# Optimization experiments

Measured on AMD Instinct MI355X. Metric: run time of the kernel, lower is better.

The kernel has to match this reference:

```python
import jax, jax.numpy as jnp
import numpy as np

N = 100000      # nodes
E = 1000000     # edges per relation
DIN = 64
DOUT = 64
NEG_SLOPE = 0.2  # DGL GATConv leaky_relu default


def setup_inputs() -> dict:
    key = jax.random.key(0)
    ks = jax.random.split(key, 16)
    inp = {"x": jax.random.normal(ks[0], (N, DIN), dtype=jnp.float32)}
    i = 1
    for rel in ("concur", "upd", "side"):
        inp[f"src_{rel}"] = jax.random.randint(ks[i], (E,), 0, N, dtype=jnp.int32); i += 1
        inp[f"dst_{rel}"] = jax.random.randint(ks[i], (E,), 0, N, dtype=jnp.int32); i += 1
        inp[f"W_{rel}"] = jax.random.normal(ks[i], (DIN, DOUT), dtype=jnp.float32) * 0.1; i += 1
        inp[f"al_{rel}"] = jax.random.normal(ks[i], (DOUT,), dtype=jnp.float32) * 0.1; i += 1
        inp[f"ar_{rel}"] = jax.random.normal(ks[i], (DOUT,), dtype=jnp.float32) * 0.1; i += 1
        inp[f"b_{rel}"] = jnp.zeros((DOUT,), dtype=jnp.float32)
    return inp


def _gat_rel(x, src, dst, W, al, ar, b, n):
    """Single-head DGL GATConv on one relation (homogeneous src/dst type)."""
    feat = x @ W                      # [N, DOUT] projected features
    el = feat @ al                    # [N] source attention logits
    er = feat @ ar                    # [N] destination attention logits
    e = el[src] + er[dst]             # [E]
    e = jnp.where(e > 0, e, NEG_SLOPE * e)  # leaky_relu
    # edge softmax normalized per destination node
    m = jax.ops.segment_max(e, dst, num_segments=n)
    a = jnp.exp(e - m[dst])
    s = jax.ops.segment_sum(a, dst, num_segments=n)
    a = a / s[dst]
    # scatter-weighted aggregation of source features onto destinations
    out = jax.ops.segment_sum(a[:, None] * feat[src], dst, num_segments=n)
    return out + b


def reference(x,
              src_concur, dst_concur, src_upd, dst_upd, src_side, dst_side,
              W_concur, al_concur, ar_concur, b_concur,
              W_upd, al_upd, ar_upd, b_upd,
              W_side, al_side, ar_side, b_side):
    n = x.shape[0]
    out = (_gat_rel(x, src_concur, dst_concur, W_concur, al_concur, ar_concur, b_concur, n)
           + _gat_rel(x, src_upd, dst_upd, W_upd, al_upd, ar_upd, b_upd, n)
           + _gat_rel(x, src_side, dst_side, W_side, al_side, ar_side, b_side, n))
    return out[:, None, :]  # [N, num_heads=1, DOUT] to match DGL GATConv output
```

## Files before the change

kernel.cpp:

```cpp
#include <hip/hip_runtime.h>

#define DIM 64
#define NEG 0.2f
#define SB 1024
#define RPW 8
#define BNODES 512
#define SHIFTB 9
#define NBMAX 1024
#define CHUNK 8192

__device__ __forceinline__ float rl(float v, int l) {
  return __int_as_float(__builtin_amdgcn_readlane(__float_as_int(v), l));
}

__device__ __forceinline__ unsigned short f2bf(float f) {
  unsigned u = __float_as_uint(f);
  u += 0x7FFFu + ((u >> 16) & 1u);
  return (unsigned short)(u >> 16);
}

__global__ __launch_bounds__(64) void prep_kernel(
    const float* __restrict__ W0, const float* __restrict__ W1, const float* __restrict__ W2,
    const float* __restrict__ al0, const float* __restrict__ ar0,
    const float* __restrict__ al1, const float* __restrict__ ar1,
    const float* __restrict__ al2, const float* __restrict__ ar2,
    const float* __restrict__ b0, const float* __restrict__ b1, const float* __restrict__ b2,
    float* __restrict__ q, float* __restrict__ bias) {
  int b = blockIdx.x, c = threadIdx.x;
  if (b < 6) {
    int rel = b >> 1;
    const float* W = rel == 0 ? W0 : (rel == 1 ? W1 : W2);
    const float* a;
    if (b & 1) a = rel == 0 ? ar0 : (rel == 1 ? ar1 : ar2);
    else       a = rel == 0 ? al0 : (rel == 1 ? al1 : al2);
    float s = 0.f;
#pragma unroll
    for (int j = 0; j < DIM; ++j) s = fmaf(W[c * DIM + j], a[j], s);
    q[b * DIM + c] = s;
  } else {
    bias[c] = b0[c] + b1[c] + b2[c];
  }
}

__global__ __launch_bounds__(256) void elr_kernel(
    const float* __restrict__ x, const float* __restrict__ q,
    float* __restrict__ el, float* __restrict__ er, int n) {
  __shared__ float Qs[6 * DIM];
  for (int i = threadIdx.x; i < 6 * DIM; i += 256) Qs[i] = q[i];
  __syncthreads();
  int i = blockIdx.x * blockDim.x + threadIdx.x;
  if (i >= n) return;
  const float4* x4 = (const float4*)x;
  const float4* Q4 = (const float4*)Qs;
  float a[6] = {0.f, 0.f, 0.f, 0.f, 0.f, 0.f};
#pragma unroll 4
  for (int t = 0; t < 16; ++t) {
    float4 xv = x4[(size_t)i * 16 + t];
#pragma unroll
    for (int j = 0; j < 6; ++j) {
      float4 qv = Q4[j * 16 + t];
      a[j] = fmaf(xv.x, qv.x, a[j]);
      a[j] = fmaf(xv.y, qv.y, a[j]);
      a[j] = fmaf(xv.z, qv.z, a[j]);
      a[j] = fmaf(xv.w, qv.w, a[j]);
    }
  }
#pragma unroll
  for (int r = 0; r < 3; ++r) {
    el[(size_t)r * n + i] = a[2 * r];
    er[(size_t)r * n + i] = a[2 * r + 1];
  }
}

__global__ __launch_bounds__(256) void proj3(
    const float* __restrict__ x,
    const float* __restrict__ W0, const float* __restrict__ W1, const float* __restrict__ W2,
    unsigned short* __restrict__ feat, int n) {
  __shared__ float WsP[3 * 4096];
  const int lane = threadIdx.x & 63;
  const int wv = threadIdx.x >> 6;
  for (int i = threadIdx.x; i < DIM * DIM; i += 256) {
    int k = i >> 6, c = i & 63;
    int d = (k >> 1) * 128 + c * 2 + (k & 1);
    WsP[d] = W0[i];
    WsP[4096 + d] = W1[i];
    WsP[8192 + d] = W2[i];
  }
  __syncthreads();

  const int rowbase = (blockIdx.x * 4 + wv) * RPW;
  float xr[RPW];
#pragma unroll
  for (int r = 0; r < RPW; ++r) {
    int row = rowbase + r;
    row = row < n ? row : n - 1;
    xr[r] = x[(size_t)row * DIM + lane];
  }
  float a0[RPW], a1[RPW], a2[RPW];
#pragma unroll
  for (int r = 0; r < RPW; ++r) { a0[r] = 0.f; a1[r] = 0.f; a2[r] = 0.f; }

  const float2* Wp0 = (const float2*)WsP;
  const float2* Wp1 = (const float2*)(WsP + 4096);
  const float2* Wp2 = (const float2*)(WsP + 8192);
#pragma unroll 8
  for (int k2 = 0; k2 < 32; ++k2) {
    float2 w0 = Wp0[k2 * 64 + lane];
    float2 w1 = Wp1[k2 * 64 + lane];
    float2 w2 = Wp2[k2 * 64 + lane];
#pragma unroll
    for (int r = 0; r < RPW; ++r) {
      float xv0 = rl(xr[r], 2 * k2);
      float xv1 = rl(xr[r], 2 * k2 + 1);
      a0[r] = fmaf(xv1, w0.y, fmaf(xv0, w0.x, a0[r]));
      a1[r] = fmaf(xv1, w1.y, fmaf(xv0, w1.x, a1[r]));
      a2[r] = fmaf(xv1, w2.y, fmaf(xv0, w2.x, a2[r]));
    }
  }
#pragma unroll
  for (int r = 0; r < RPW; ++r) {
    int row = rowbase + r;
    if (row < n) {
      feat[(size_t)row * DIM + lane] = f2bf(a0[r]);
      feat[((size_t)n + row) * DIM + lane] = f2bf(a1[r]);
      feat[((size_t)2 * n + row) * DIM + lane] = f2bf(a2[r]);
    }
  }
}

__global__ __launch_bounds__(256) void proj_kernel(
    const float* __restrict__ x, const float* __restrict__ W,
    const float* __restrict__ al, const float* __restrict__ ar,
    unsigned short* __restrict__ feat, float* __restrict__ el, float* __restrict__ er, int n) {
  __shared__ float Ws[DIM][DIM];
  int tid = threadIdx.y * 64 + threadIdx.x;
  for (int i = tid; i < DIM * DIM; i += 256) Ws[i >> 6][i & 63] = W[i];
  __syncthreads();
  int row = blockIdx.x * 4 + threadIdx.y;
  if (row >= n) return;
  int lane = threadIdx.x;
  const float* xr = x + (size_t)row * DIM;
  float acc = 0.f;
#pragma unroll
  for (int k = 0; k < DIM; ++k) acc = fmaf(xr[k], Ws[k][lane], acc);
  feat[(size_t)row * DIM + lane] = f2bf(acc);
  float pl = acc * al[lane], pr = acc * ar[lane];
#pragma unroll
  for (int o = 32; o > 0; o >>= 1) {
    pl += __shfl_xor(pl, o, 64);
    pr += __shfl_xor(pr, o, 64);
  }
  if (lane == 0) { el[row] = pl; er[row] = pr; }
}

__global__ void init_out(float* __restrict__ out,
                         const float* __restrict__ b0, const float* __restrict__ b1,
                         const float* __restrict__ b2, int n) {
  int i = blockIdx.x * blockDim.x + threadIdx.x;
  if (i < n * DIM) {
    int c = i & (DIM - 1);
    out[i] = b0[c] + b1[c] + b2[c];
  }
}

__global__ void count3(const int* __restrict__ d0, const int* __restrict__ d1,
                       const int* __restrict__ d2, int e0, int e1, int e2,
                       int* __restrict__ cnt, int n) {
  int i = blockIdx.x * blockDim.x + threadIdx.x;
  int r, li;
  const int* dp;
  if (i < e0)                { r = 0; li = i;           dp = d0; }
  else if (i < e0 + e1)      { r = 1; li = i - e0;      dp = d1; }
  else if (i < e0 + e1 + e2) { r = 2; li = i - e0 - e1; dp = d2; }
  else return;
  atomicAdd(&cnt[r * n + dp[li]], 1);
}

__global__ __launch_bounds__(SB) void scan1(const int* __restrict__ cnt, int* __restrict__ off,
                                            int* __restrict__ bsum, int n) {
  __shared__ int sm[SB];
  int i = blockIdx.x * SB + threadIdx.x;
  int v = (i < n) ? cnt[i] : 0;
  sm[threadIdx.x] = v;
  __syncthreads();
  for (int o = 1; o < SB; o <<= 1) {
    int t = ((int)threadIdx.x >= o) ? sm[threadIdx.x - o] : 0;
    __syncthreads();
    sm[threadIdx.x] += t;
    __syncthreads();
  }
  if (i < n) off[i + 1] = sm[threadIdx.x];
  if (threadIdx.x == SB - 1) bsum[blockIdx.x] = sm[SB - 1];
}

__global__ __launch_bounds__(SB) void scan2(int* __restrict__ bsum, int nb) {
  __shared__ int sm[SB];
  int v = ((int)threadIdx.x < nb) ? bsum[threadIdx.x] : 0;
  sm[threadIdx.x] = v;
  __syncthreads();
  for (int o = 1; o < SB; o <<= 1) {
    int t = ((int)threadIdx.x >= o) ? sm[threadIdx.x - o] : 0;
    __syncthreads();
    sm[threadIdx.x] += t;
    __syncthreads();
  }
  if ((int)threadIdx.x < nb) bsum[threadIdx.x] = sm[threadIdx.x] - v;
}

__global__ __launch_bounds__(SB) void scan3(int* __restrict__ off, const int* __restrict__ bsum,
                                            int n) {
  int i = blockIdx.x * SB + threadIdx.x;
  if (i < n) off[i + 1] += bsum[blockIdx.x];
  if (i == 0) off[0] = 0;
}

__global__ void init_bcur(const int* __restrict__ off, int* __restrict__ bcur, int nbuckets) {
  int b = blockIdx.x * blockDim.x + threadIdx.x;
  if (b < nbuckets) bcur[b] = off[b << SHIFTB];
}

__global__ __launch_bounds__(256) void bin3(
    const int* __restrict__ s0, const int* __restrict__ d0,
    const int* __restrict__ s1, const int* __restrict__ d1,
    const int* __restrict__ s2, const int* __restrict__ d2,
    int e0, int e1, int e2,
    const float* __restrict__ el, const float* __restrict__ er,
    int* __restrict__ bcur, int2* __restrict__ binPairs,
    unsigned short* __restrict__ binLoc, int n, int nbuckets) {
  __shared__ int hist[NBMAX];
  __shared__ int base[NBMAX];
  const int tot = e0 + e1 + e2;
  const int cbeg = blockIdx.x * CHUNK;
  const int cend = min(cbeg + CHUNK, tot);
  for (int b = threadIdx.x; b < nbuckets; b += 256) hist[b] = 0;
  __syncthreads();
  for (int i = cbeg + threadIdx.x; i < cend; i += 256) {
    int r, li;
    const int* dp;
    if (i < e0)           { r = 0; li = i;           dp = d0; }
    else if (i < e0 + e1) { r = 1; li = i - e0;      dp = d1; }
    else                  { r = 2; li = i - e0 - e1; dp = d2; }
    atomicAdd(&hist[(r * n + dp[li]) >> SHIFTB], 1);
  }
  __syncthreads();
  for (int b = threadIdx.x; b < nbuckets; b += 256) {
    int h = hist[b];
    base[b] = h ? atomicAdd(&bcur[b], h) : 0;
    hist[b] = 0;
  }
  __syncthreads();
  for (int i = cbeg + threadIdx.x; i < cend; i += 256) {
    int r, li;
    const int *sp, *dp;
    if (i < e0)           { r = 0; li = i;           sp = s0; dp = d0; }
    else if (i < e0 + e1) { r = 1; li = i - e0;      sp = s1; dp = d1; }
    else                  { r = 2; li = i - e0 - e1; sp = s2; dp = d2; }
    int d = dp[li], sN = sp[li];
    int gi = r * n + d;
    int b = gi >> SHIFTB;
    float v = el[(size_t)r * n + sN] + er[gi];
    v = v > 0.f ? v : NEG * v;
    int slot = atomicAdd(&hist[b], 1);
    int idx = base[b] + slot;
    int2 pr;
    pr.x = sN;
    pr.y = __float_as_int(v);
    binPairs[idx] = pr;
    binLoc[idx] = (unsigned short)(gi - (b << SHIFTB));
  }
}

__global__ __launch_bounds__(256) void place(
    const int* __restrict__ off, const int2* __restrict__ binPairs,
    const unsigned short* __restrict__ binLoc, int* __restrict__ cur,
    int2* __restrict__ pairs, int m) {
  const int b = blockIdx.x;
  const int gbeg = b << SHIFTB;
  const int gend = min(gbeg + BNODES, m);
  const int beg = off[gbeg], end = off[gend];
  for (int i = beg + threadIdx.x; i < end; i += 256) {
    int2 pr = binPairs[i];
    int gi = gbeg + (int)binLoc[i];
    int p = atomicAdd(&cur[gi], 1);
    pairs[off[gi] + p] = pr;
  }
}

__global__ void scatter_pair(const int* __restrict__ src, const int* __restrict__ dst,
                             const float* __restrict__ el, const float* __restrict__ er,
                             const int* __restrict__ off_r, int* __restrict__ cur_r,
                             int2* __restrict__ pairs, int ebase, int e) {
  int i = blockIdx.x * blockDim.x + threadIdx.x;
  if (i < e) {
    int d = dst[i], sN = src[i];
    float v = el[sN] + er[d];
    v = v > 0.f ? v : NEG * v;
    int p = atomicAdd(&cur_r[d], 1);
    int2 pr;
    pr.x = sN;
    pr.y = __float_as_int(v);
    pairs[off_r[d] + p - ebase] = pr;
  }
}

__device__ __forceinline__ float2 rel2(const unsigned* __restrict__ fu,
                                       const int2* __restrict__ pairs,
                                       int beg, int end, int hl, int sl) {
  float2 acc = make_float2(0.f, 0.f);
  int deg = end - beg;
  if (deg <= 0) return acc;
  const int lbase = hl << 5;
  float s;
  if (deg <= 32) {
    int2 pr = (sl < deg) ? pairs[beg + sl] : make_int2(0, 0xFF800000);
    float v = __int_as_float(pr.y);
    float m = v;
#pragma unroll
    for (int o = 16; o > 0; o >>= 1) m = fmaxf(m, __shfl_xor(m, o, 64));
    float a = (sl < deg) ? __expf(v - m) : 0.f;
    float t = a;
#pragma unroll
    for (int o = 16; o > 0; o >>= 1) t += __shfl_xor(t, o, 64);
    s = t;
    int j = 0, bulk = deg & ~3;
    for (; j < bulk; j += 4) {
      int sn0 = __shfl(pr.x, lbase + j, 64);     float a0 = __shfl(a, lbase + j, 64);
      int sn1 = __shfl(pr.x, lbase + j + 1, 64); float a1 = __shfl(a, lbase + j + 1, 64);
      int sn2 = __shfl(pr.x, lbase + j + 2, 64); float a2 = __shfl(a, lbase + j + 2, 64);
      int sn3 = __shfl(pr.x, lbase + j + 3, 64); float a3 = __shfl(a, lbase + j + 3, 64);
      unsigned u0 = fu[((size_t)sn0 << 5) + sl];
      unsigned u1 = fu[((size_t)sn1 << 5) + sl];
      unsigned u2 = fu[((size_t)sn2 << 5) + sl];
      unsigned u3 = fu[((size_t)sn3 << 5) + sl];
      acc.x = fmaf(a0, __uint_as_float(u0 << 16), acc.x);
      acc.y = fmaf(a0, __uint_as_float(u0 & 0xFFFF0000u), acc.y);
      acc.x = fmaf(a1, __uint_as_float(u1 << 16), acc.x);
      acc.y = fmaf(a1, __uint_as_float(u1 & 0xFFFF0000u), acc.y);
      acc.x = fmaf(a2, __uint_as_float(u2 << 16), acc.x);
      acc.y = fmaf(a2, __uint_as_float(u2 & 0xFFFF0000u), acc.y);
      acc.x = fmaf(a3, __uint_as_float(u3 << 16), acc.x);
      acc.y = fmaf(a3, __uint_as_float(u3 & 0xFFFF0000u), acc.y);
    }
    for (; j < deg; ++j) {
      int sn = __shfl(pr.x, lbase + j, 64);
      float aj = __shfl(a, lbase + j, 64);
      unsigned u = fu[((size_t)sn << 5) + sl];
      acc.x = fmaf(aj, __uint_as_float(u << 16), acc.x);
      acc.y = fmaf(aj, __uint_as_float(u & 0xFFFF0000u), acc.y);
    }
  } else {
    float m = -3.4e38f;
    for (int i = beg + sl; i < end; i += 32) m = fmaxf(m, __int_as_float(pairs[i].y));
#pragma unroll
    for (int o = 16; o > 0; o >>= 1) m = fmaxf(m, __shfl_xor(m, o, 64));
    s = 0.f;
    for (int base = beg; base < end; base += 32) {
      int cm = min(32, end - base);
      int2 pr = (sl < cm) ? pairs[base + sl] : make_int2(0, 0);
      float a = (sl < cm) ? __expf(__int_as_float(pr.y) - m) : 0.f;
      float t = a;
#pragma unroll
      for (int o = 16; o > 0; o >>= 1) t += __shfl_xor(t, o, 64);
      s += t;
      for (int j = 0; j < cm; ++j) {
        int sn = __shfl(pr.x, lbase + j, 64);
        float aj = __shfl(a, lbase + j, 64);
        unsigned u = fu[((size_t)sn << 5) + sl];
        acc.x = fmaf(aj, __uint_as_float(u << 16), acc.x);
        acc.y = fmaf(aj, __uint_as_float(u & 0xFFFF0000u), acc.y);
      }
    }
  }
  acc.x /= s;
  acc.y /= s;
  return acc;
}

__global__ __launch_bounds__(256) void agg3(
    const unsigned* __restrict__ fu, const int* __restrict__ off,
    const int2* __restrict__ pairs, const float* __restrict__ bias,
    float* __restrict__ out, int n) {
  int wave = (blockIdx.x * blockDim.x + threadIdx.x) >> 6;
  int lane = threadIdx.x & 63;
  int hl = lane >> 5, sl = lane & 31;
  int node = (wave << 1) + hl;
  if (node >= n) return;
  int o0b = off[node],         o0e = off[node + 1];
  int o1b = off[n + node],     o1e = off[n + node + 1];
  int o2b = off[2 * n + node], o2e = off[2 * n + node + 1];
  int c0 = sl << 1;
  float2 r = *(const float2*)(bias + c0);
  float2 c;
  c = rel2(fu, pairs, o0b, o0e, hl, sl);
  r.x += c.x; r.y += c.y;
  c = rel2(fu + (size_t)n * 32, pairs, o1b, o1e, hl, sl);
  r.x += c.x; r.y += c.y;
  c = rel2(fu + (size_t)2 * n * 32, pairs, o2b, o2e, hl, sl);
  r.x += c.x; r.y += c.y;
  *(float2*)(out + ((size_t)node << 6) + c0) = r;
}

__global__ __launch_bounds__(256) void agg1(
    const unsigned* __restrict__ fu, const int* __restrict__ off_r,
    const int2* __restrict__ pairs, int ebase, float* __restrict__ out, int n) {
  int wave = (blockIdx.x * blockDim.x + threadIdx.x) >> 6;
  int lane = threadIdx.x & 63;
  int hl = lane >> 5, sl = lane & 31;
  int node = (wave << 1) + hl;
  if (node >= n) return;
  float2 c = rel2(fu, pairs, off_r[node] - ebase, off_r[node + 1] - ebase, hl, sl);
  float* op = out + ((size_t)node << 6) + (sl << 1);
  op[0] += c.x;
  op[1] += c.y;
}

static inline char* alignup(char* p) {
  return (char*)(((uintptr_t)p + 255) & ~(uintptr_t)255);
}

extern "C" void kernel_launch(void* const* d_in, const int* in_sizes, int n_in,
                              void* d_out, int out_size, void* d_ws, size_t ws_size,
                              hipStream_t stream) {
  const float* x = (const float*)d_in[0];
  const int n = in_sizes[0] / DIM;
  const int m = 3 * n;
  float* out = (float*)d_out;

  const int eN[3] = {in_sizes[1], in_sizes[7], in_sizes[13]};
  const int eTot = eN[0] + eN[1] + eN[2];
  const int nbuckets = (m + BNODES - 1) >> SHIFTB;

  const size_t featB = (size_t)n * DIM * sizeof(unsigned short);
  const size_t nB = (size_t)n * sizeof(float);

  const size_t needFused = 3 * featB + 6 * nB + 2 * (size_t)m * 4 + (size_t)(m + 2) * 4 +
                           SB * 4 + 448 * 4 + NBMAX * 4 + (size_t)eTot * 8 +
                           (size_t)eTot * 8 + (size_t)eTot * 2 + 64 * 256;
  const bool fused = (ws_size >= needFused) && (nbuckets <= NBMAX);

  char* w = (char*)d_ws;
  unsigned short* feat = (unsigned short*)w;
  w += fused ? 3 * featB : featB;                      w = alignup(w);
  float* el = (float*)w;    w += fused ? 3 * nB : nB;  w = alignup(w);
  float* er = (float*)w;    w += fused ? 3 * nB : nB;  w = alignup(w);
  int* cnt = (int*)w;       w += (size_t)m * 4;
  int* cur = (int*)w;       w += (size_t)m * 4;        w = alignup(w);
  int* off = (int*)w;       w += (size_t)(m + 1) * 4;  w = alignup(w);
  int* bsum = (int*)w;      w += SB * 4;               w = alignup(w);
  float* qbuf = (float*)w;  w += 384 * 4;
  float* bias = (float*)w;  w += 64 * 4;               w = alignup(w);
  int* bcur = (int*)w;      w += NBMAX * 4;            w = alignup(w);
  int2* pairs = (int2*)w;   w += (size_t)eTot * 8;     w = alignup(w);
  int2* binPairs = (int2*)w; w += (size_t)eTot * 8;    w = alignup(w);
  unsigned short* binLoc = (unsigned short*)w;

  const int nb = (m + SB - 1) / SB;

  hipMemsetAsync(cnt, 0, (size_t)2 * m * sizeof(int), stream);
  count3<<<(eTot + 255) / 256, 256, 0, stream>>>(
      (const int*)d_in[2], (const int*)d_in[8], (const int*)d_in[14],
      eN[0], eN[1], eN[2], cnt, n);
  scan1<<<nb, SB, 0, stream>>>(cnt, off, bsum, m);
  scan2<<<1, SB, 0, stream>>>(bsum, nb);
  scan3<<<nb, SB, 0, stream>>>(off, bsum, m);

  if (fused) {
    prep_kernel<<<7, 64, 0, stream>>>(
        (const float*)d_in[3], (const float*)d_in[9], (const float*)d_in[15],
        (const float*)d_in[4], (const float*)d_in[5],
        (const float*)d_in[10], (const float*)d_in[11],
        (const float*)d_in[16], (const float*)d_in[17],
        (const float*)d_in[6], (const float*)d_in[12], (const float*)d_in[18],
        qbuf, bias);
    elr_kernel<<<(n + 255) / 256, 256, 0, stream>>>(x, qbuf, el, er, n);
    proj3<<<(n + 4 * RPW - 1) / (4 * RPW), 256, 0, stream>>>(
        x, (const float*)d_in[3], (const float*)d_in[9], (const float*)d_in[15], feat, n);
    init_bcur<<<(nbuckets + 255) / 256, 256, 0, stream>>>(off, bcur, nbuckets);
    bin3<<<(eTot + CHUNK - 1) / CHUNK, 256, 0, stream>>>(
        (const int*)d_in[1], (const int*)d_in[2], (const int*)d_in[7], (const int*)d_in[8],
        (const int*)d_in[13], (const int*)d_in[14], eN[0], eN[1], eN[2],
        el, er, bcur, binPairs, binLoc, n, nbuckets);
    place<<<nbuckets, 256, 0, stream>>>(off, binPairs, binLoc, cur, pairs, m);
    agg3<<<(n + 7) / 8, 256, 0, stream>>>((const unsigned*)feat, off, pairs, bias, out, n);
  } else {
    init_out<<<(n * DIM + 255) / 256, 256, 0, stream>>>(
        out, (const float*)d_in[6], (const float*)d_in[12], (const float*)d_in[18], n);
    int ebase = 0;
    for (int r = 0; r < 3; ++r) {
      const int base = 1 + r * 6;
      proj_kernel<<<(n + 3) / 4, dim3(64, 4), 0, stream>>>(
          x, (const float*)d_in[base + 2], (const float*)d_in[base + 3],
          (const float*)d_in[base + 4], feat, el, er, n);
      scatter_pair<<<(eN[r] + 255) / 256, 256, 0, stream>>>(
          (const int*)d_in[base], (const int*)d_in[base + 1], el, er, off + (size_t)r * n,
          cur + (size_t)r * n, pairs, ebase, eN[r]);
      agg1<<<(n + 7) / 8, 256, 0, stream>>>((const unsigned*)feat, off + (size_t)r * n,
                                            pairs, ebase, out, n);
      ebase += eN[r];
    }
  }
}
```

Baseline: 611.6 us.

## Replace global place pass with per-bucket LDS CSR build and aggregation

Edge logits are now computed once per edge in the counting pass and stored. Binning uses 1024-node buckets with LDS staging and coalesced writes. The separate place kernel and global CSR pairs array are gone: each aggregation block rebuilds its bucket's CSR in shared memory and runs the softmax-weighted gather from LDS, adding into a bias-initialised output with atomics. This drops one full edge-array pass through global memory, at the cost of float atomics on the output and a slow fallback for overflowing buckets.

```diff
diff --git a/kernel.cpp b/kernel.cpp
--- a/kernel.cpp
+++ b/kernel.cpp
@@ -4,15 +4,15 @@
 #define NEG 0.2f
 #define SB 1024
 #define RPW 8
-#define BNODES 512
-#define SHIFTB 9
-#define NBMAX 1024
+#define SHIFTB 10
+#define BN 1024
+#define NB2 512
 #define CHUNK 8192
+#define CAP 16384
 
 __device__ __forceinline__ float rl(float v, int l) {
   return __int_as_float(__builtin_amdgcn_readlane(__float_as_int(v), l));
 }
-
 __device__ __forceinline__ unsigned short f2bf(float f) {
   unsigned u = __float_as_uint(f);
   u += 0x7FFFu + ((u >> 16) & 1u);
@@ -24,22 +24,17 @@
     const float* __restrict__ al0, const float* __restrict__ ar0,
     const float* __restrict__ al1, const float* __restrict__ ar1,
     const float* __restrict__ al2, const float* __restrict__ ar2,
-    const float* __restrict__ b0, const float* __restrict__ b1, const float* __restrict__ b2,
-    float* __restrict__ q, float* __restrict__ bias) {
+    float* __restrict__ q) {
   int b = blockIdx.x, c = threadIdx.x;
-  if (b < 6) {
-    int rel = b >> 1;
-    const float* W = rel == 0 ? W0 : (rel == 1 ? W1 : W2);
-    const float* a;
-    if (b & 1) a = rel == 0 ? ar0 : (rel == 1 ? ar1 : ar2);
-    else       a = rel == 0 ? al0 : (rel == 1 ? al1 : al2);
-    float s = 0.f;
-#pragma unroll
-    for (int j = 0; j < DIM; ++j) s = fmaf(W[c * DIM + j], a[j], s);
-    q[b * DIM + c] = s;
-  } else {
-    bias[c] = b0[c] + b1[c] + b2[c];
-  }
+  int rel = b >> 1;
+  const float* W = rel == 0 ? W0 : (rel == 1 ? W1 : W2);
+  const float* a;
+  if (b & 1) a = rel == 0 ? ar0 : (rel == 1 ? ar1 : ar2);
+  else       a = rel == 0 ? al0 : (rel == 1 ? al1 : al2);
+  float s = 0.f;
+#pragma unroll
+  for (int j = 0; j < DIM; ++j) s = fmaf(W[c * DIM + j], a[j], s);
+  q[b * DIM + c] = s;
 }
 
 __global__ __launch_bounds__(256) void elr_kernel(
@@ -87,7 +82,6 @@
     WsP[8192 + d] = W2[i];
   }
   __syncthreads();
-
   const int rowbase = (blockIdx.x * 4 + wv) * RPW;
   float xr[RPW];
 #pragma unroll
@@ -99,7 +93,6 @@
   float a0[RPW], a1[RPW], a2[RPW];
 #pragma unroll
   for (int r = 0; r < RPW; ++r) { a0[r] = 0.f; a1[r] = 0.f; a2[r] = 0.f; }
-
   const float2* Wp0 = (const float2*)WsP;
   const float2* Wp1 = (const float2*)(WsP + 4096);
   const float2* Wp2 = (const float2*)(WsP + 8192);
@@ -128,6 +121,279 @@
   }
 }
 
+__global__ void init_out(float* __restrict__ out,
+                         const float* __restrict__ b0, const float* __restrict__ b1,
+                         const float* __restrict__ b2, int n) {
+  int i = blockIdx.x * blockDim.x + threadIdx.x;
+  if (i < n * DIM) {
+    int c = i & (DIM - 1);
+    out[i] = b0[c] + b1[c] + b2[c];
+  }
+}
+
+__global__ void edgev_kernel(const int* __restrict__ s0, const int* __restrict__ d0,
+                             const int* __restrict__ s1, const int* __restrict__ d1,
+                             const int* __restrict__ s2, const int* __restrict__ d2,
+                             int e0, int e1, int e2,
+                             const float* __restrict__ el, const float* __restrict__ er,
+                             float* __restrict__ ve, int* __restrict__ cnt, int n) {
+  int i = blockIdx.x * blockDim.x + threadIdx.x;
+  int r, li;
+  const int *sp, *dp;
+  if (i < e0)                { r = 0; li = i;           sp = s0; dp = d0; }
+  else if (i < e0 + e1)      { r = 1; li = i - e0;      sp = s1; dp = d1; }
+  else if (i < e0 + e1 + e2) { r = 2; li = i - e0 - e1; sp = s2; dp = d2; }
+  else return;
+  int sN = sp[li], gi = r * n + dp[li];
+  float v = el[(size_t)r * n + sN] + er[gi];
+  v = v > 0.f ? v : NEG * v;
+  ve[i] = v;
+  atomicAdd(&cnt[gi], 1);
+}
+
+__global__ __launch_bounds__(SB) void scan1(const int* __restrict__ cnt, int* __restrict__ off,
+                                            int* __restrict__ bsum, int n) {
+  __shared__ int sm[SB];
+  int i = blockIdx.x * SB + threadIdx.x;
+  int v = (i < n) ? cnt[i] : 0;
+  sm[threadIdx.x] = v;
+  __syncthreads();
+  for (int o = 1; o < SB; o <<= 1) {
+    int t = ((int)threadIdx.x >= o) ? sm[threadIdx.x - o] : 0;
+    __syncthreads();
+    sm[threadIdx.x] += t;
+    __syncthreads();
+  }
+  if (i < n) off[i + 1] = sm[threadIdx.x];
+  if (threadIdx.x == SB - 1) bsum[blockIdx.x] = sm[SB - 1];
+}
+__global__ __launch_bounds__(SB) void scan2(int* __restrict__ bsum, int nb) {
+  __shared__ int sm[SB];
+  int v = ((int)threadIdx.x < nb) ? bsum[threadIdx.x] : 0;
+  sm[threadIdx.x] = v;
+  __syncthreads();
+  for (int o = 1; o < SB; o <<= 1) {
+    int t = ((int)threadIdx.x >= o) ? sm[threadIdx.x - o] : 0;
+    __syncthreads();
+    sm[threadIdx.x] += t;
+    __syncthreads();
+  }
+  if ((int)threadIdx.x < nb) bsum[threadIdx.x] = sm[threadIdx.x] - v;
+}
+__global__ __launch_bounds__(SB) void scan3(int* __restrict__ off, const int* __restrict__ bsum,
+                                            int n) {
+  int i = blockIdx.x * SB + threadIdx.x;
+  if (i < n) off[i + 1] += bsum[blockIdx.x];
+  if (i == 0) off[0] = 0;
+}
+
+__global__ void init_bcur(const int* __restrict__ off, int* __restrict__ bcur, int nbuckets) {
+  int b = blockIdx.x * blockDim.x + threadIdx.x;
+  if (b < nbuckets) bcur[b] = off[b << SHIFTB];
+}
+
+__global__ __launch_bounds__(512) void binb(
+    const int* __restrict__ s0, const int* __restrict__ d0,
+    const int* __restrict__ s1, const int* __restrict__ d1,
+    const int* __restrict__ s2, const int* __restrict__ d2,
+    int e0, int e1, int e2, const float* __restrict__ ve,
+    int* __restrict__ bcur, int2* __restrict__ binPairs, int n, int nbuckets) {
+  __shared__ int hist[NB2], lbase[NB2], gbase[NB2], lcur[NB2];
+  __shared__ int2 stage[CHUNK];
+  const int tot = e0 + e1 + e2;
+  const int cbeg = blockIdx.x * CHUNK;
+  const int cend = min(cbeg + CHUNK, tot);
+  const int tid = threadIdx.x;
+  for (int b = tid; b < NB2; b += 512) hist[b] = 0;
+  __syncthreads();
+  for (int i = cbeg + tid; i < cend; i += 512) {
+    int r, li;
+    const int* dp;
+    if (i < e0)           { r = 0; li = i;           dp = d0; }
+    else if (i < e0 + e1) { r = 1; li = i - e0;      dp = d1; }
+    else                  { r = 2; li = i - e0 - e1; dp = d2; }
+    atomicAdd(&hist[(r * n + dp[li]) >> SHIFTB], 1);
+  }
+  __syncthreads();
+  lbase[tid] = hist[tid];
+  __syncthreads();
+  for (int o = 1; o < NB2; o <<= 1) {
+    int t = (tid >= o) ? lbase[tid - o] : 0;
+    __syncthreads();
+    lbase[tid] += t;
+    __syncthreads();
+  }
+  {
+    int h = hist[tid];
+    lbase[tid] -= h;
+    gbase[tid] = h ? atomicAdd(&bcur[tid], h) : 0;
+    lcur[tid] = 0;
+  }
+  __syncthreads();
+  for (int i = cbeg + tid; i < cend; i += 512) {
+    int r, li;
+    const int *sp, *dp;
+    if (i < e0)           { r = 0; li = i;           sp = s0; dp = d0; }
+    else if (i < e0 + e1) { r = 1; li = i - e0;      sp = s1; dp = d1; }
+    else                  { r = 2; li = i - e0 - e1; sp = s2; dp = d2; }
+    int gi = r * n + dp[li];
+    int b = gi >> SHIFTB;
+    int slot = lbase[b] + atomicAdd(&lcur[b], 1);
+    int2 rec;
+    rec.x = ((gi & (BN - 1)) << 17) | sp[li];
+    rec.y = __float_as_int(ve[i]);
+    stage[slot] = rec;
+  }
+  __syncthreads();
+  const int wid = tid >> 6, lane = tid & 63;
+  for (int b = wid; b < nbuckets; b += 8) {
+    int h = hist[b], lb = lbase[b], gb = gbase[b];
+    for (int k = lane; k < h; k += 64) binPairs[gb + k] = stage[lb + k];
+  }
+}
+
+__device__ __forceinline__ float2 rel2_lds(const int2* __restrict__ csr,
+                                           const unsigned* __restrict__ fu,
+                                           int b0, int b1, int lb, int sl) {
+  float2 acc = make_float2(0.f, 0.f);
+  int deg = b1 - b0;
+  float s;
+  if (deg <= 32) {
+    int2 pr = (sl < deg) ? csr[b0 + sl] : make_int2(0, 0xFF800000);
+    float v = __int_as_float(pr.y);
+    float m = v;
+#pragma unroll
+    for (int o = 16; o > 0; o >>= 1) m = fmaxf(m, __shfl_xor(m, o, 64));
+    float a = (sl < deg) ? __expf(v - m) : 0.f;
+    float t = a;
+#pragma unroll
+    for (int o = 16; o > 0; o >>= 1) t += __shfl_xor(t, o, 64);
+    s = t;
+    int j = 0, bulk = deg & ~3;
+    for (; j < bulk; j += 4) {
+      int x0 = __shfl(pr.x, lb + j, 64);     float a0 = __shfl(a, lb + j, 64);
+      int x1 = __shfl(pr.x, lb + j + 1, 64); float a1 = __shfl(a, lb + j + 1, 64);
+      int x2 = __shfl(pr.x, lb + j + 2, 64); float a2 = __shfl(a, lb + j + 2, 64);
+      int x3 = __shfl(pr.x, lb + j + 3, 64); float a3 = __shfl(a, lb + j + 3, 64);
+      unsigned u0 = fu[((size_t)(x0 & 0x1FFFF) << 5) + sl];
+      unsigned u1 = fu[((size_t)(x1 & 0x1FFFF) << 5) + sl];
+      unsigned u2 = fu[((size_t)(x2 & 0x1FFFF) << 5) + sl];
+      unsigned u3 = fu[((size_t)(x3 & 0x1FFFF) << 5) + sl];
+      acc.x = fmaf(a0, __uint_as_float(u0 << 16), acc.x);
+      acc.y = fmaf(a0, __uint_as_float(u0 & 0xFFFF0000u), acc.y);
+      acc.x = fmaf(a1, __uint_as_float(u1 << 16), acc.x);
+      acc.y = fmaf(a1, __uint_as_float(u1 & 0xFFFF0000u), acc.y);
+      acc.x = fmaf(a2, __uint_as_float(u2 << 16), acc.x);
+      acc.y = fmaf(a2, __uint_as_float(u2 & 0xFFFF0000u), acc.y);
+      acc.x = fmaf(a3, __uint_as_float(u3 << 16), acc.x);
+      acc.y = fmaf(a3, __uint_as_float(u3 & 0xFFFF0000u), acc.y);
+    }
+    for (; j < deg; ++j) {
+      int xx = __shfl(pr.x, lb + j, 64);
+      float aj = __shfl(a, lb + j, 64);
+      unsigned u = fu[((size_t)(xx & 0x1FFFF) << 5) + sl];
+      acc.x = fmaf(aj, __uint_as_float(u << 16), acc.x);
+      acc.y = fmaf(aj, __uint_as_float(u & 0xFFFF0000u), acc.y);
+    }
+  } else {
+    float m = -3.4e38f;
+    for (int i = b0 + sl; i < b1; i += 32) m = fmaxf(m, __int_as_float(csr[i].y));
+#pragma unroll
+    for (int o = 16; o > 0; o >>= 1) m = fmaxf(m, __shfl_xor(m, o, 64));
+    s = 0.f;
+    for (int base = b0; base < b1; base += 32) {
+      int cm = min(32, b1 - base);
+      int2 pr = (sl < cm) ? csr[base + sl] : make_int2(0, 0);
+      float a = (sl < cm) ? __expf(__int_as_float(pr.y) - m) : 0.f;
+      float t = a;
+#pragma unroll
+      for (int o = 16; o > 0; o >>= 1) t += __shfl_xor(t, o, 64);
+      s += t;
+      for (int j = 0; j < cm; ++j) {
+        int xx = __shfl(pr.x, lb + j, 64);
+        float aj = __shfl(a, lb + j, 64);
+        unsigned u = fu[((size_t)(xx & 0x1FFFF) << 5) + sl];
+        acc.x = fmaf(aj, __uint_as_float(u << 16), acc.x);
+        acc.y = fmaf(aj, __uint_as_float(u & 0xFFFF0000u), acc.y);
+      }
+    }
+  }
+  acc.x /= s;
+  acc.y /= s;
+  return acc;
+}
+
+__global__ __launch_bounds__(512) void aggb(
+    const unsigned* __restrict__ fu, const int* __restrict__ off,
+    const int2* __restrict__ binPairs, float* __restrict__ out, int n, int m) {
+  __shared__ int soff[BN + 1];
+  __shared__ int lcur[BN];
+  __shared__ int2 csr[CAP];
+  const int gbeg = blockIdx.x << SHIFTB;
+  const int gend = min(gbeg + BN, m);
+  const int ng = gend - gbeg;
+  const int tid = threadIdx.x;
+  for (int t = tid; t <= ng; t += 512) soff[t] = off[gbeg + t];
+  for (int t = tid; t < ng; t += 512) lcur[t] = 0;
+  __syncthreads();
+  const int base = soff[0];
+  const int total = soff[ng] - base;
+  const int lane = tid & 63, sl = tid & 31, hw = tid >> 5, lb = lane & 32;
+
+  if (total <= CAP) {
+    for (int i = base + tid; i < base + total; i += 512) {
+      int2 e = binPairs[i];
+      int loc = ((unsigned)e.x) >> 17;
+      int slot = soff[loc] - base + atomicAdd(&lcur[loc], 1);
+      csr[slot] = e;
+    }
+    __syncthreads();
+    for (int ln = hw; ln < ng; ln += 16) {
+      int c0 = soff[ln] - base, c1 = soff[ln + 1] - base;
+      if (c1 == c0) continue;
+      int gi = gbeg + ln;
+      int r = gi >= 2 * n ? 2 : (gi >= n ? 1 : 0);
+      int d = gi - r * n;
+      float2 res = rel2_lds(csr, fu + (size_t)r * n * 32, c0, c1, lb, sl);
+      atomicAdd(&out[(size_t)d * DIM + 2 * sl], res.x);
+      atomicAdd(&out[(size_t)d * DIM + 2 * sl + 1], res.y);
+    }
+  } else {
+    for (int ln = hw; ln < ng; ln += 16) {
+      if (soff[ln + 1] == soff[ln]) continue;
+      int gi = gbeg + ln;
+      int r = gi >= 2 * n ? 2 : (gi >= n ? 1 : 0);
+      int d = gi - r * n;
+      const unsigned* fr = fu + (size_t)r * n * 32;
+      float mx = -3.4e38f;
+      for (int i = base + sl; i < base + total; i += 32) {
+        int2 e = binPairs[i];
+        if ((int)(((unsigned)e.x) >> 17) == ln) mx = fmaxf(mx, __int_as_float(e.y));
+      }
+#pragma unroll
+      for (int o = 16; o > 0; o >>= 1) mx = fmaxf(mx, __shfl_xor(mx, o, 64));
+      float s = 0.f;
+      for (int i = base + sl; i < base + total; i += 32) {
+        int2 e = binPairs[i];
+        if ((int)(((unsigned)e.x) >> 17) == ln) s += __expf(__int_as_float(e.y) - mx);
+      }
+#pragma unroll
+      for (int o = 16; o > 0; o >>= 1) s += __shfl_xor(s, o, 64);
+      float2 acc = make_float2(0.f, 0.f);
+      for (int i = base; i < base + total; ++i) {
+        int2 e = binPairs[i];
+        if ((int)(((unsigned)e.x) >> 17) != ln) continue;
+        float a = __expf(__int_as_float(e.y) - mx);
+        unsigned u = fr[((size_t)(e.x & 0x1FFFF) << 5) + sl];
+        acc.x = fmaf(a, __uint_as_float(u << 16), acc.x);
+        acc.y = fmaf(a, __uint_as_float(u & 0xFFFF0000u), acc.y);
+      }
+      atomicAdd(&out[(size_t)d * DIM + 2 * sl], acc.x / s);
+      atomicAdd(&out[(size_t)d * DIM + 2 * sl + 1], acc.y / s);
+    }
+  }
+}
+
 __global__ __launch_bounds__(256) void proj_kernel(
     const float* __restrict__ x, const float* __restrict__ W,
     const float* __restrict__ al, const float* __restrict__ ar,
@@ -153,137 +419,9 @@
   if (lane == 0) { el[row] = pl; er[row] = pr; }
 }
 
-__global__ void init_out(float* __restrict__ out,
-                         const float* __restrict__ b0, const float* __restrict__ b1,
-                         const float* __restrict__ b2, int n) {
+__global__ void count1(const int* __restrict__ dst, int* __restrict__ cnt, int e) {
   int i = blockIdx.x * blockDim.x + threadIdx.x;
-  if (i < n * DIM) {
-    int c = i & (DIM - 1);
-    out[i] = b0[c] + b1[c] + b2[c];
-  }
-}
-
-__global__ void count3(const int* __restrict__ d0, const int* __restrict__ d1,
-                       const int* __restrict__ d2, int e0, int e1, int e2,
-                       int* __restrict__ cnt, int n) {
-  int i = blockIdx.x * blockDim.x + threadIdx.x;
-  int r, li;
-  const int* dp;
-  if (i < e0)                { r = 0; li = i;           dp = d0; }
-  else if (i < e0 + e1)      { r = 1; li = i - e0;      dp = d1; }
-  else if (i < e0 + e1 + e2) { r = 2; li = i - e0 - e1; dp = d2; }
-  else return;
-  atomicAdd(&cnt[r * n + dp[li]], 1);
-}
-
-__global__ __launch_bounds__(SB) void scan1(const int* __restrict__ cnt, int* __restrict__ off,
-                                            int* __restrict__ bsum, int n) {
-  __shared__ int sm[SB];
-  int i = blockIdx.x * SB + threadIdx.x;
-  int v = (i < n) ? cnt[i] : 0;
-  sm[threadIdx.x] = v;
-  __syncthreads();
-  for (int o = 1; o < SB; o <<= 1) {
-    int t = ((int)threadIdx.x >= o) ? sm[threadIdx.x - o] : 0;
-    __syncthreads();
-    sm[threadIdx.x] += t;
-    __syncthreads();
-  }
-  if (i < n) off[i + 1] = sm[threadIdx.x];
-  if (threadIdx.x == SB - 1) bsum[blockIdx.x] = sm[SB - 1];
-}
-
-__global__ __launch_bounds__(SB) void scan2(int* __restrict__ bsum, int nb) {
-  __shared__ int sm[SB];
-  int v = ((int)threadIdx.x < nb) ? bsum[threadIdx.x] : 0;
-  sm[threadIdx.x] = v;
-  __syncthreads();
-  for (int o = 1; o < SB; o <<= 1) {
-    int t = ((int)threadIdx.x >= o) ? sm[threadIdx.x - o] : 0;
-    __syncthreads();
-    sm[threadIdx.x] += t;
-    __syncthreads();
-  }
-  if ((int)threadIdx.x < nb) bsum[threadIdx.x] = sm[threadIdx.x] - v;
-}
-
-__global__ __launch_bounds__(SB) void scan3(int* __restrict__ off, const int* __restrict__ bsum,
-                                            int n) {
-  int i = blockIdx.x * SB + threadIdx.x;
-  if (i < n) off[i + 1] += bsum[blockIdx.x];
-  if (i == 0) off[0] = 0;
-}
-
-__global__ void init_bcur(const int* __restrict__ off, int* __restrict__ bcur, int nbuckets) {
-  int b = blockIdx.x * blockDim.x + threadIdx.x;
-  if (b < nbuckets) bcur[b] = off[b << SHIFTB];
-}
-
-__global__ __launch_bounds__(256) void bin3(
-    const int* __restrict__ s0, const int* __restrict__ d0,
-    const int* __restrict__ s1, const int* __restrict__ d1,
-    const int* __restrict__ s2, const int* __restrict__ d2,
-    int e0, int e1, int e2,
-    const float* __restrict__ el, const float* __restrict__ er,
-    int* __restrict__ bcur, int2* __restrict__ binPairs,
-    unsigned short* __restrict__ binLoc, int n, int nbuckets) {
-  __shared__ int hist[NBMAX];
-  __shared__ int base[NBMAX];
-  const int tot = e0 + e1 + e2;
-  const int cbeg = blockIdx.x * CHUNK;
-  const int cend = min(cbeg + CHUNK, tot);
-  for (int b = threadIdx.x; b < nbuckets; b += 256) hist[b] = 0;
-  __syncthreads();
-  for (int i = cbeg + threadIdx.x; i < cend; i += 256) {
-    int r, li;
-    const int* dp;
-    if (i < e0)           { r = 0; li = i;           dp = d0; }
-    else if (i < e0 + e1) { r = 1; li = i - e0;      dp = d1; }
-    else                  { r = 2; li = i - e0 - e1; dp = d2; }
-    atomicAdd(&hist[(r * n + dp[li]) >> SHIFTB], 1);
-  }
-  __syncthreads();
-  for (int b = threadIdx.x; b < nbuckets; b += 256) {
-    int h = hist[b];
-    base[b] = h ? atomicAdd(&bcur[b], h) : 0;
-    hist[b] = 0;
-  }
-  __syncthreads();
-  for (int i = cbeg + threadIdx.x; i < cend; i += 256) {
-    int r, li;
-    const int *sp, *dp;
-    if (i < e0)           { r = 0; li = i;           sp = s0; dp = d0; }
-    else if (i < e0 + e1) { r = 1; li = i - e0;      sp = s1; dp = d1; }
-    else                  { r = 2; li = i - e0 - e1; sp = s2; dp = d2; }
-    int d = dp[li], sN = sp[li];
-    int gi = r * n + d;
-    int b = gi >> SHIFTB;
-    float v = el[(size_t)r * n + sN] + er[gi];
-    v = v > 0.f ? v : NEG * v;
-    int slot = atomicAdd(&hist[b], 1);
-    int idx = base[b] + slot;
-    int2 pr;
-    pr.x = sN;
-    pr.y = __float_as_int(v);
-    binPairs[idx] = pr;
-    binLoc[idx] = (unsigned short)(gi - (b << SHIFTB));
-  }
-}
-
-__global__ __launch_bounds__(256) void place(
-    const int* __restrict__ off, const int2* __restrict__ binPairs,
-    const unsigned short* __restrict__ binLoc, int* __restrict__ cur,
-    int2* __restrict__ pairs, int m) {
-  const int b = blockIdx.x;
-  const int gbeg = b << SHIFTB;
-  const int gend = min(gbeg + BNODES, m);
-  const int beg = off[gbeg], end = off[gend];
-  for (int i = beg + threadIdx.x; i < end; i += 256) {
-    int2 pr = binPairs[i];
-    int gi = gbeg + (int)binLoc[i];
-    int p = atomicAdd(&cur[gi], 1);
-    pairs[off[gi] + p] = pr;
-  }
+  if (i < e) atomicAdd(&cnt[dst[i]], 1);
 }
 
 __global__ void scatter_pair(const int* __restrict__ src, const int* __restrict__ dst,
@@ -303,9 +441,9 @@
   }
 }
 
-__device__ __forceinline__ float2 rel2(const unsigned* __restrict__ fu,
-                                       const int2* __restrict__ pairs,
-                                       int beg, int end, int hl, int sl) {
+__device__ __forceinline__ float2 rel2g(const unsigned* __restrict__ fu,
+                                        const int2* __restrict__ pairs,
+                                        int beg, int end, int hl, int sl) {
   float2 acc = make_float2(0.f, 0.f);
   int deg = end - beg;
   if (deg <= 0) return acc;
@@ -322,26 +460,7 @@
 #pragma unroll
     for (int o = 16; o > 0; o >>= 1) t += __shfl_xor(t, o, 64);
     s = t;
-    int j = 0, bulk = deg & ~3;
-    for (; j < bulk; j += 4) {
-      int sn0 = __shfl(pr.x, lbase + j, 64);     float a0 = __shfl(a, lbase + j, 64);
-      int sn1 = __shfl(pr.x, lbase + j + 1, 64); float a1 = __shfl(a, lbase + j + 1, 64);
-      int sn2 = __shfl(pr.x, lbase + j + 2, 64); float a2 = __shfl(a, lbase + j + 2, 64);
-      int sn3 = __shfl(pr.x, lbase + j + 3, 64); float a3 = __shfl(a, lbase + j + 3, 64);
-      unsigned u0 = fu[((size_t)sn0 << 5) + sl];
-      unsigned u1 = fu[((size_t)sn1 << 5) + sl];
-      unsigned u2 = fu[((size_t)sn2 << 5) + sl];
-      unsigned u3 = fu[((size_t)sn3 << 5) + sl];
-      acc.x = fmaf(a0, __uint_as_float(u0 << 16), acc.x);
-      acc.y = fmaf(a0, __uint_as_float(u0 & 0xFFFF0000u), acc.y);
-      acc.x = fmaf(a1, __uint_as_float(u1 << 16), acc.x);
-      acc.y = fmaf(a1, __uint_as_float(u1 & 0xFFFF0000u), acc.y);
-      acc.x = fmaf(a2, __uint_as_float(u2 << 16), acc.x);
-      acc.y = fmaf(a2, __uint_as_float(u2 & 0xFFFF0000u), acc.y);
-      acc.x = fmaf(a3, __uint_as_float(u3 << 16), acc.x);
-      acc.y = fmaf(a3, __uint_as_float(u3 & 0xFFFF0000u), acc.y);
-    }
-    for (; j < deg; ++j) {
+    for (int j = 0; j < deg; ++j) {
       int sn = __shfl(pr.x, lbase + j, 64);
       float aj = __shfl(a, lbase + j, 64);
       unsigned u = fu[((size_t)sn << 5) + sl];
@@ -376,30 +495,6 @@
   return acc;
 }
 
-__global__ __launch_bounds__(256) void agg3(
-    const unsigned* __restrict__ fu, const int* __restrict__ off,
-    const int2* __restrict__ pairs, const float* __restrict__ bias,
-    float* __restrict__ out, int n) {
-  int wave = (blockIdx.x * blockDim.x + threadIdx.x) >> 6;
-  int lane = threadIdx.x & 63;
-  int hl = lane >> 5, sl = lane & 31;
-  int node = (wave << 1) + hl;
-  if (node >= n) return;
-  int o0b = off[node],         o0e = off[node + 1];
-  int o1b = off[n + node],     o1e = off[n + node + 1];
-  int o2b = off[2 * n + node], o2e = off[2 * n + node + 1];
-  int c0 = sl << 1;
-  float2 r = *(const float2*)(bias + c0);
-  float2 c;
-  c = rel2(fu, pairs, o0b, o0e, hl, sl);
-  r.x += c.x; r.y += c.y;
-  c = rel2(fu + (size_t)n * 32, pairs, o1b, o1e, hl, sl);
-  r.x += c.x; r.y += c.y;
-  c = rel2(fu + (size_t)2 * n * 32, pairs, o2b, o2e, hl, sl);
-  r.x += c.x; r.y += c.y;
-  *(float2*)(out + ((size_t)node << 6) + c0) = r;
-}
-
 __global__ __launch_bounds__(256) void agg1(
     const unsigned* __restrict__ fu, const int* __restrict__ off_r,
     const int2* __restrict__ pairs, int ebase, float* __restrict__ out, int n) {
@@ -408,7 +503,7 @@
   int hl = lane >> 5, sl = lane & 31;
   int node = (wave << 1) + hl;
   if (node >= n) return;
-  float2 c = rel2(fu, pairs, off_r[node] - ebase, off_r[node + 1] - ebase, hl, sl);
+  float2 c = rel2g(fu, pairs, off_r[node] - ebase, off_r[node + 1] - ebase, hl, sl);
   float* op = out + ((size_t)node << 6) + (sl << 1);
   op[0] += c.x;
   op[1] += c.y;
@@ -428,15 +523,15 @@
 
   const int eN[3] = {in_sizes[1], in_sizes[7], in_sizes[13]};
   const int eTot = eN[0] + eN[1] + eN[2];
-  const int nbuckets = (m + BNODES - 1) >> SHIFTB;
+  const int nbuckets = (m + BN - 1) >> SHIFTB;
 
   const size_t featB = (size_t)n * DIM * sizeof(unsigned short);
   const size_t nB = (size_t)n * sizeof(float);
 
   const size_t needFused = 3 * featB + 6 * nB + 2 * (size_t)m * 4 + (size_t)(m + 2) * 4 +
-                           SB * 4 + 448 * 4 + NBMAX * 4 + (size_t)eTot * 8 +
-                           (size_t)eTot * 8 + (size_t)eTot * 2 + 64 * 256;
-  const bool fused = (ws_size >= needFused) && (nbuckets <= NBMAX);
+                           SB * 4 + 384 * 4 + NB2 * 4 + (size_t)eTot * 4 +
+                           (size_t)eTot * 8 + 64 * 256;
+  const bool fused = (ws_size >= needFused) && (nbuckets <= NB2) && (n <= 131072);
 
   char* w = (char*)d_ws;
   unsigned short* feat = (unsigned short*)w;
@@ -447,42 +542,46 @@
   int* cur = (int*)w;       w += (size_t)m * 4;        w = alignup(w);
   int* off = (int*)w;       w += (size_t)(m + 1) * 4;  w = alignup(w);
   int* bsum = (int*)w;      w += SB * 4;               w = alignup(w);
-  float* qbuf = (float*)w;  w += 384 * 4;
-  float* bias = (float*)w;  w += 64 * 4;               w = alignup(w);
-  int* bcur = (int*)w;      w += NBMAX * 4;            w = alignup(w);
-  int2* pairs = (int2*)w;   w += (size_t)eTot * 8;     w = alignup(w);
-  int2* binPairs = (int2*)w; w += (size_t)eTot * 8;    w = alignup(w);
-  unsigned short* binLoc = (unsigned short*)w;
+  float* qbuf = (float*)w;  w += 384 * 4;              w = alignup(w);
+  int* bcur = (int*)w;      w += NB2 * 4;              w = alignup(w);
+  float* ve = (float*)w;    w += (size_t)eTot * 4;     w = alignup(w);
+  int2* binPairs = (int2*)w;
 
   const int nb = (m + SB - 1) / SB;
 
-  hipMemsetAsync(cnt, 0, (size_t)2 * m * sizeof(int), stream);
-  count3<<<(eTot + 255) / 256, 256, 0, stream>>>(
-      (const int*)d_in[2], (const int*)d_in[8], (const int*)d_in[14],
-      eN[0], eN[1], eN[2], cnt, n);
-  scan1<<<nb, SB, 0, stream>>>(cnt, off, bsum, m);
-  scan2<<<1, SB, 0, stream>>>(bsum, nb);
-  scan3<<<nb, SB, 0, stream>>>(off, bsum, m);
-
   if (fused) {
-    prep_kernel<<<7, 64, 0, stream>>>(
+    hipMemsetAsync(cnt, 0, (size_t)m * sizeof(int), stream);
+    prep_kernel<<<6, 64, 0, stream>>>(
         (const float*)d_in[3], (const float*)d_in[9], (const float*)d_in[15],
         (const float*)d_in[4], (const float*)d_in[5],
         (const float*)d_in[10], (const float*)d_in[11],
-        (const float*)d_in[16], (const float*)d_in[17],
-        (const float*)d_in[6], (const float*)d_in[12], (const float*)d_in[18],
-        qbuf, bias);
+        (const float*)d_in[16], (const float*)d_in[17], qbuf);
     elr_kernel<<<(n + 255) / 256, 256, 0, stream>>>(x, qbuf, el, er, n);
+    edgev_kernel<<<(eTot + 255) / 256, 256, 0, stream>>>(
+        (const int*)d_in[1], (const int*)d_in[2], (const int*)d_in[7], (const int*)d_in[8],
+        (const int*)d_in[13], (const int*)d_in[14], eN[0], eN[1], eN[2],
+        el, er, ve, cnt, n);
+    scan1<<<nb, SB, 0, stream>>>(cnt, off, bsum, m);
+    scan2<<<1, SB, 0, stream>>>(bsum, nb);
+    scan3<<<nb, SB, 0, stream>>>(off, bsum, m);
     proj3<<<(n + 4 * RPW - 1) / (4 * RPW), 256, 0, stream>>>(
         x, (const float*)d_in[3], (const float*)d_in[9], (const float*)d_in[15], feat, n);
     init_bcur<<<(nbuckets + 255) / 256, 256, 0, stream>>>(off, bcur, nbuckets);
-    bin3<<<(eTot + CHUNK - 1) / CHUNK, 256, 0, stream>>>(
+    binb<<<(eTot + CHUNK - 1) / CHUNK, 512, 0, stream>>>(
         (const int*)d_in[1], (const int*)d_in[2], (const int*)d_in[7], (const int*)d_in[8],
         (const int*)d_in[13], (const int*)d_in[14], eN[0], eN[1], eN[2],
-        el, er, bcur, binPairs, binLoc, n, nbuckets);
-    place<<<nbuckets, 256, 0, stream>>>(off, binPairs, binLoc, cur, pairs, m);
-    agg3<<<(n + 7) / 8, 256, 0, stream>>>((const unsigned*)feat, off, pairs, bias, out, n);
+        ve, bcur, binPairs, n, nbuckets);
+    init_out<<<(n * DIM + 255) / 256, 256, 0, stream>>>(
+        out, (const float*)d_in[6], (const float*)d_in[12], (const float*)d_in[18], n);
+    aggb<<<nbuckets, 512, 0, stream>>>((const unsigned*)feat, off, binPairs, out, n, m);
   } else {
+    hipMemsetAsync(cnt, 0, (size_t)2 * m * sizeof(int), stream);
+    for (int r = 0; r < 3; ++r)
+      count1<<<(eN[r] + 255) / 256, 256, 0, stream>>>((const int*)d_in[2 + 6 * r],
+                                                      cnt + (size_t)r * n, eN[r]);
+    scan1<<<nb, SB, 0, stream>>>(cnt, off, bsum, m);
+    scan2<<<1, SB, 0, stream>>>(bsum, nb);
+    scan3<<<nb, SB, 0, stream>>>(off, bsum, m);
     init_out<<<(n * DIM + 255) / 256, 256, 0, stream>>>(
         out, (const float*)d_in[6], (const float*)d_in[12], (const float*)d_in[18], n);
     int ebase = 0;
@@ -493,9 +592,9 @@
           (const float*)d_in[base + 4], feat, el, er, n);
       scatter_pair<<<(eN[r] + 255) / 256, 256, 0, stream>>>(
           (const int*)d_in[base], (const int*)d_in[base + 1], el, er, off + (size_t)r * n,
-          cur + (size_t)r * n, pairs, ebase, eN[r]);
+          cur + (size_t)r * n, binPairs, ebase, eN[r]);
       agg1<<<(n + 7) / 8, 256, 0, stream>>>((const unsigned*)feat, off + (size_t)r * n,
-                                            pairs, ebase, out, n);
+                                            binPairs, ebase, out, n);
       ebase += eN[r];
     }
   }
```

After: 685.3 us. 1.12x slower.
